# Performance work log

Hardware: AMD Instinct MI355X
Metric: run time of the kernel (lower is better)

The kernel has to match this reference:

```python
import jax, jax.numpy as jnp
import numpy as np

ALPHA = 0.2  # leaky relu negative slope (LinearNet default)


def _init_linear(key, fan_in, fan_out):
    kw, kb = jax.random.split(key)
    lim = 1.0 / np.sqrt(fan_in)
    W = jax.random.uniform(kw, (fan_in, fan_out), jnp.float32, -lim, lim)
    b = jax.random.uniform(kb, (fan_out,), jnp.float32, -lim, lim)
    return W, b


def setup_inputs() -> dict:
    key = jax.random.key(0)
    keys = jax.random.split(key, 8)
    B, N, F = 8, 512, 32
    x = jax.random.normal(keys[0], (B, N, F), jnp.float32)
    # fe: [2F=64 -> 64 -> 64 -> 64], all layers leaky-relu (final_linear=False)
    fe_W0, fe_b0 = _init_linear(keys[1], 2 * F, 64)
    fe_W1, fe_b1 = _init_linear(keys[2], 64, 64)
    fe_W2, fe_b2 = _init_linear(keys[3], 64, 64)
    # fn: [64 + F = 96 -> 128 -> 128 -> 32], last layer linear (final_linear=True)
    fn_W0, fn_b0 = _init_linear(keys[4], 64 + F, 128)
    fn_W1, fn_b1 = _init_linear(keys[5], 128, 128)
    fn_W2, fn_b2 = _init_linear(keys[6], 128, 32)
    return {
        "x": x,
        "fe_W0": fe_W0, "fe_b0": fe_b0,
        "fe_W1": fe_W1, "fe_b1": fe_b1,
        "fe_W2": fe_W2, "fe_b2": fe_b2,
        "fn_W0": fn_W0, "fn_b0": fn_b0,
        "fn_W1": fn_W1, "fn_b1": fn_b1,
        "fn_W2": fn_W2, "fn_b2": fn_b2,
    }


def reference(x, fe_W0, fe_b0, fe_W1, fe_b1, fe_W2, fe_b2,
              fn_W0, fn_b0, fn_W1, fn_b1, fn_W2, fn_b2):
    B, N, F = x.shape
    # all-pairs edge inputs: A[b,i,j] = concat(x[b,i], x[b,j])  (x1=repeat rows, x2=tile)
    xi = jnp.broadcast_to(x[:, :, None, :], (B, N, N, F))
    xj = jnp.broadcast_to(x[:, None, :, :], (B, N, N, F))
    A = jnp.concatenate([xi, xj], axis=-1)  # [B, N, N, 2F]
    # edge MLP fe: leaky relu after every layer (final_linear=False)
    for W, b in ((fe_W0, fe_b0), (fe_W1, fe_b1), (fe_W2, fe_b2)):
        A = jax.nn.leaky_relu(A @ W + b, negative_slope=ALPHA)
    # sum aggregation over the sender axis j
    agg = jnp.sum(A, axis=2)  # [B, N, K]
    h = jnp.concatenate([agg, x], axis=-1)  # [B, N, K + F]
    # node MLP fn: leaky relu on hidden layers, final layer linear
    h = jax.nn.leaky_relu(h @ fn_W0 + fn_b0, negative_slope=ALPHA)
    h = jax.nn.leaky_relu(h @ fn_W1 + fn_b1, negative_slope=ALPHA)
    out = h @ fn_W2 + fn_b2  # [B, N, output_node_size]
    return out
```

## Files before the change

### kernel.cpp

```cpp
#include <hip/hip_runtime.h>
#include <hip/hip_bf16.h>

#define ALPHA 0.2f
static __device__ __forceinline__ float lrel(float x) { return fmaxf(x, ALPHA * x); }

typedef __attribute__((ext_vector_type(8))) short bf16x8;
typedef __attribute__((ext_vector_type(4))) float f32x4;

union FragU { bf16x8 v; unsigned int u[4]; uint4 q; };

static __device__ __forceinline__ unsigned int pk2(float a, float b) {
    unsigned int r;
    asm("v_cvt_pk_bf16_f32 %0, %1, %2" : "=v"(r) : "v"(a), "v"(b));
    return r;
}
static __device__ __forceinline__ unsigned int cvl2(float a, float b) {
    return pk2(lrel(a), lrel(b));
}
static __device__ __forceinline__ unsigned short f2bf(float x) {
    union { float f; unsigned int u; } c;
    c.f = x;
    unsigned int r = c.u + 0x7FFFu + ((c.u >> 16) & 1u);
    return (unsigned short)(r >> 16);
}
static __device__ __forceinline__ int pi64(int s) {
    return 32 * ((s >> 4) >> 1) + 8 * ((s >> 2) & 3) + 4 * ((s >> 4) & 1) + (s & 3);
}

__global__ __launch_bounds__(256) void k_uv(
    const float* __restrict__ x, const float* __restrict__ W0, const float* __restrict__ b0,
    const float* __restrict__ W1, const float* __restrict__ W2,
    float* __restrict__ Upi, unsigned short* __restrict__ xbf, unsigned int* __restrict__ WF)
{
    if (blockIdx.x == 1024) {
        const int t = threadIdx.x;
        const int l = t & 63, part = t >> 6;
        const int lo = l & 15, g = l >> 4;
        for (int ff = part; ff < 20; ff += 4) {
            unsigned int o[4];
            if (ff < 4) {
                const int nf = ff;
                const int pc = 32 * (nf >> 1) + 8 * (lo >> 2) + 4 * (nf & 1) + (lo & 3);
#pragma unroll
                for (int uq = 0; uq < 4; ++uq) {
                    const int k0 = 8 * g + 2 * uq;
                    o[uq] = pk2(W0[(32 + k0) * 64 + pc], W0[(33 + k0) * 64 + pc]);
                }
            } else if (ff < 12) {
                const int s = (ff - 4) >> 2, nf = (ff - 4) & 3;
                const int pc = 32 * (nf >> 1) + 8 * (lo >> 2) + 4 * (nf & 1) + (lo & 3);
#pragma unroll
                for (int uq = 0; uq < 4; ++uq) {
                    const int k0 = 32 * s + 8 * g + 2 * uq;
                    o[uq] = pk2(W1[k0 * 64 + pc], W1[(k0 + 1) * 64 + pc]);
                }
            } else {
                const int s = (ff - 12) >> 2, nf = (ff - 12) & 3;
                const int c2 = 16 * nf + lo;
#pragma unroll
                for (int uq = 0; uq < 4; ++uq) {
                    const int k0 = 32 * s + 8 * g + 2 * uq;
                    o[uq] = pk2(W2[k0 * 64 + c2], W2[(k0 + 1) * 64 + c2]);
                }
            }
            *(uint4*)(WF + (ff * 64 + l) * 4) = make_uint4(o[0], o[1], o[2], o[3]);
        }
        return;
    }
    const int idx = blockIdx.x * 256 + threadIdx.x;
    const int n = idx >> 6;
    const int slot = idx & 63;
    const int f = pi64(slot);
    const float* xr = x + n * 32;
    float u = b0[f];
#pragma unroll
    for (int i = 0; i < 32; ++i) u += xr[i] * W0[i * 64 + f];
    Upi[idx] = u;
    if (slot < 32) xbf[n * 32 + slot] = f2bf(xr[slot]);
}

__global__ __launch_bounds__(256, 3) void k_edge(
    const float* __restrict__ Upi, const unsigned short* __restrict__ xbf,
    const unsigned int* __restrict__ WF,
    const float* __restrict__ b1, const float* __restrict__ b2,
    float* __restrict__ AGG)
{
    __shared__ uint4 wlds[1024];
    const int tid = threadIdx.x;
    const int w = tid >> 6, l = tid & 63;
    const int lo = l & 15, g = l >> 4;
    const int bid = blockIdx.x;
    const int b = bid >> 7, ig = bid & 127;
    const int node = b * 512 + ig * 4 + w;

    for (int idx = tid; idx < 1024; idx += 256)
        wlds[idx] = ((const uint4*)WF)[256 + idx];

    FragU w0f[4];
    const uint4* wp = (const uint4*)WF;
#pragma unroll
    for (int nf = 0; nf < 4; ++nf) w0f[nf].q = wp[nf * 64 + l];

    f32x4 u0f[4], b1f[4], b2f[4];
#pragma unroll
    for (int nf = 0; nf < 4; ++nf) {
        const float4 t0 = *(const float4*)(Upi + node * 64 + nf * 16 + 4 * g);
        u0f[nf] = (f32x4){t0.x, t0.y, t0.z, t0.w};
        const float4 t1 = *(const float4*)(b1 + 32 * (nf >> 1) + 8 * g + 4 * (nf & 1));
        const float4 t2 = *(const float4*)(b2 + 16 * nf + 4 * g);
        b1f[nf] = (f32x4){t1.x, t1.y, t1.z, t1.w};
        b2f[nf] = (f32x4){t2.x, t2.y, t2.z, t2.w};
    }

    const unsigned short* xb = xbf + b * 512 * 32;

    FragU xjT0, xjB;
    xjT0.q = *(const uint4*)(xb + lo * 32 + 8 * g);
    xjB.q  = *(const uint4*)(xb + (16 + lo) * 32 + 8 * g);

    __syncthreads();

    f32x4 acc0c[4];
#pragma unroll
    for (int nf = 0; nf < 4; ++nf)
        acc0c[nf] = __builtin_amdgcn_mfma_f32_16x16x32_bf16(w0f[nf].v, xjT0.v, u0f[nf], 0, 0, 0);

    f32x4 acc2p[4];
#pragma unroll
    for (int nf = 0; nf < 4; ++nf) { f32x4 z = {0.f, 0.f, 0.f, 0.f}; acc2p[nf] = z; }

    float aggL[4][4];
#pragma unroll
    for (int nf = 0; nf < 4; ++nf)
#pragma unroll
        for (int r = 0; r < 4; ++r) aggL[nf][r] = 0.f;

#pragma unroll 2
    for (int k = 0; k < 32; ++k) {
        int widx = 0;
        asm volatile("" : "+v"(widx));

        const int jn = ((k + 2) & 31) * 16;
        FragU xjn;
        xjn.q = *(const uint4*)(xb + (jn + lo) * 32 + 8 * g);

        __builtin_amdgcn_s_setprio(1);
        f32x4 acc0n[4];
#pragma unroll
        for (int nf = 0; nf < 4; ++nf)
            acc0n[nf] = __builtin_amdgcn_mfma_f32_16x16x32_bf16(w0f[nf].v, xjB.v, u0f[nf], 0, 0, 0);
        __builtin_amdgcn_s_setprio(0);

        FragU q0, q1;
        q0.u[0] = cvl2(acc0c[0][0], acc0c[0][1]);
        q0.u[1] = cvl2(acc0c[0][2], acc0c[0][3]);
        q0.u[2] = cvl2(acc0c[1][0], acc0c[1][1]);
        q0.u[3] = cvl2(acc0c[1][2], acc0c[1][3]);
        q1.u[0] = cvl2(acc0c[2][0], acc0c[2][1]);
        q1.u[1] = cvl2(acc0c[2][2], acc0c[2][3]);
        q1.u[2] = cvl2(acc0c[3][0], acc0c[3][1]);
        q1.u[3] = cvl2(acc0c[3][2], acc0c[3][3]);

        __builtin_amdgcn_s_setprio(1);
        f32x4 acc1[4];
#pragma unroll
        for (int nf = 0; nf < 4; ++nf) {
            FragU wa, wb;
            wa.q = wlds[widx + nf * 64 + l];
            wb.q = wlds[widx + (4 + nf) * 64 + l];
            acc1[nf] = __builtin_amdgcn_mfma_f32_16x16x32_bf16(wa.v, q0.v, b1f[nf], 0, 0, 0);
            acc1[nf] = __builtin_amdgcn_mfma_f32_16x16x32_bf16(wb.v, q1.v, acc1[nf], 0, 0, 0);
        }
        __builtin_amdgcn_s_setprio(0);

#pragma unroll
        for (int nf = 0; nf < 4; ++nf)
#pragma unroll
            for (int r = 0; r < 4; ++r) aggL[nf][r] += lrel(acc2p[nf][r]);

        FragU p0, p1;
        p0.u[0] = cvl2(acc1[0][0], acc1[0][1]);
        p0.u[1] = cvl2(acc1[0][2], acc1[0][3]);
        p0.u[2] = cvl2(acc1[1][0], acc1[1][1]);
        p0.u[3] = cvl2(acc1[1][2], acc1[1][3]);
        p1.u[0] = cvl2(acc1[2][0], acc1[2][1]);
        p1.u[1] = cvl2(acc1[2][2], acc1[2][3]);
        p1.u[2] = cvl2(acc1[3][0], acc1[3][1]);
        p1.u[3] = cvl2(acc1[3][2], acc1[3][3]);

        __builtin_amdgcn_s_setprio(1);
#pragma unroll
        for (int nf = 0; nf < 4; ++nf) {
            FragU wa, wb;
            wa.q = wlds[widx + (8 + nf) * 64 + l];
            wb.q = wlds[widx + (12 + nf) * 64 + l];
            acc2p[nf] = __builtin_amdgcn_mfma_f32_16x16x32_bf16(wa.v, p0.v, b2f[nf], 0, 0, 0);
            acc2p[nf] = __builtin_amdgcn_mfma_f32_16x16x32_bf16(wb.v, p1.v, acc2p[nf], 0, 0, 0);
        }
        __builtin_amdgcn_s_setprio(0);

#pragma unroll
        for (int nf = 0; nf < 4; ++nf) acc0c[nf] = acc0n[nf];
        xjB = xjn;
    }

#pragma unroll
    for (int nf = 0; nf < 4; ++nf)
#pragma unroll
        for (int r = 0; r < 4; ++r) aggL[nf][r] += lrel(acc2p[nf][r]);

#pragma unroll
    for (int nf = 0; nf < 4; ++nf)
#pragma unroll
        for (int r = 0; r < 4; ++r) {
            float v = aggL[nf][r];
            v += __shfl_xor(v, 1);
            v += __shfl_xor(v, 2);
            v += __shfl_xor(v, 4);
            v += __shfl_xor(v, 8);
            aggL[nf][r] = v;
        }
    if (lo == 0) {
#pragma unroll
        for (int nf = 0; nf < 4; ++nf) {
            float4 o = {aggL[nf][0], aggL[nf][1], aggL[nf][2], aggL[nf][3]};
            *(float4*)(AGG + node * 64 + 16 * nf + 4 * g) = o;
        }
    }
}

__global__ __launch_bounds__(256) void k_fn(
    const float* __restrict__ AGG, const float* __restrict__ x,
    const float* __restrict__ W0, const float* __restrict__ b0,
    const float* __restrict__ W1, const float* __restrict__ b1,
    const float* __restrict__ W2, const float* __restrict__ b2,
    float* __restrict__ out)
{
    __shared__ float in96T[96][8];
    __shared__ float h1T[128][8];
    __shared__ float h2T[128][8];
    const int t = threadIdx.x;
    const int half = t >> 7, f = t & 127;
    const int node0 = blockIdx.x * 8;

    for (int idx = t; idx < 768; idx += 256) {
        int nn = idx & 7, k = idx >> 3;
        in96T[k][nn] = (k < 64) ? AGG[(node0 + nn) * 64 + k]
                                : x[(node0 + nn) * 32 + (k - 64)];
    }
    __syncthreads();

    {
        float a0 = b0[f], a1 = a0, a2 = a0, a3 = a0;
#pragma unroll 4
        for (int k = 0; k < 96; ++k) {
            const float4 iv = *(const float4*)(&in96T[k][4 * half]);
            const float wv = W0[k * 128 + f];
            a0 += iv.x * wv; a1 += iv.y * wv; a2 += iv.z * wv; a3 += iv.w * wv;
        }
        float4 o = {lrel(a0), lrel(a1), lrel(a2), lrel(a3)};
        *(float4*)(&h1T[f][4 * half]) = o;
    }
    __syncthreads();

    {
        float a0 = b1[f], a1 = a0, a2 = a0, a3 = a0;
#pragma unroll 4
        for (int k = 0; k < 128; ++k) {
            const float4 iv = *(const float4*)(&h1T[k][4 * half]);
            const float wv = W1[k * 128 + f];
            a0 += iv.x * wv; a1 += iv.y * wv; a2 += iv.z * wv; a3 += iv.w * wv;
        }
        float4 o = {lrel(a0), lrel(a1), lrel(a2), lrel(a3)};
        *(float4*)(&h2T[f][4 * half]) = o;
    }
    __syncthreads();

    {
        const int nn = t >> 5, fo = t & 31;
        float a = b2[fo];
#pragma unroll 4
        for (int k = 0; k < 128; ++k) a += h2T[k][nn] * W2[k * 32 + fo];
        out[(node0 + nn) * 32 + fo] = a;
    }
}

extern "C" void kernel_launch(void* const* d_in, const int* in_sizes, int n_in,
                              void* d_out, int out_size, void* d_ws, size_t ws_size,
                              hipStream_t stream)
{
    const float* x    = (const float*)d_in[0];
    const float* feW0 = (const float*)d_in[1];
    const float* feb0 = (const float*)d_in[2];
    const float* feW1 = (const float*)d_in[3];
    const float* feb1 = (const float*)d_in[4];
    const float* feW2 = (const float*)d_in[5];
    const float* feb2 = (const float*)d_in[6];
    const float* fnW0 = (const float*)d_in[7];
    const float* fnb0 = (const float*)d_in[8];
    const float* fnW1 = (const float*)d_in[9];
    const float* fnb1 = (const float*)d_in[10];
    const float* fnW2 = (const float*)d_in[11];
    const float* fnb2 = (const float*)d_in[12];
    float* out = (float*)d_out;

    float* Upi = (float*)d_ws;
    float* AGG = Upi + 262144;
    unsigned short* xbf = (unsigned short*)(AGG + 262144);
    unsigned int* WF = (unsigned int*)(xbf + 131072);

    hipLaunchKernelGGL(k_uv,   dim3(1025), dim3(256), 0, stream, x, feW0, feb0, feW1, feW2, Upi, xbf, WF);
    hipLaunchKernelGGL(k_edge, dim3(1024), dim3(256), 0, stream, Upi, xbf, WF, feb1, feb2, AGG);
    hipLaunchKernelGGL(k_fn,   dim3(512),  dim3(256), 0, stream, AGG, x, fnW0, fnb0, fnW1, fnb1, fnW2, fnb2, out);
}
```

Measured before the change: 81.27 us.

## Interleave two j-tiles per iteration with inline-asm MFMA and fused leaky-relu aggregation

Restructures the edge loop to process two 16-wide sender tiles (A and B) per iteration, interleaving their MFMA chains so independent matrix ops hide each other's latency. The previous software pipeline (layer-0 MFMA one tile ahead, layer-2 activation one iteration behind) is dropped. MFMAs are now issued through inline asm with explicit accumulate constraints, and the leaky-relu sum is rewritten as 0.6x + 0.4|x| via two FMAs. Occupancy drops from 3 to 2 blocks per SM to make room for the extra live registers, and inline asm may limit how the compiler schedules instructions.

```diff
diff --git a/kernel.cpp b/kernel.cpp
--- a/kernel.cpp
+++ b/kernel.cpp
@@ -8,6 +8,15 @@
 typedef __attribute__((ext_vector_type(4))) float f32x4;
 
 union FragU { bf16x8 v; unsigned int u[4]; uint4 q; };
+
+static __device__ __forceinline__ f32x4 mfma_init(bf16x8 a, bf16x8 b, f32x4 c) {
+    f32x4 d;
+    asm("v_mfma_f32_16x16x32_bf16 %0, %1, %2, %3" : "=&v"(d) : "v"(a), "v"(b), "v"(c));
+    return d;
+}
+static __device__ __forceinline__ void mfma_acc(f32x4& acc, bf16x8 a, bf16x8 b) {
+    asm("v_mfma_f32_16x16x32_bf16 %0, %1, %2, %0" : "+v"(acc) : "v"(a), "v"(b));
+}
 
 static __device__ __forceinline__ unsigned int pk2(float a, float b) {
     unsigned int r;
@@ -16,6 +25,9 @@
 }
 static __device__ __forceinline__ unsigned int cvl2(float a, float b) {
     return pk2(lrel(a), lrel(b));
+}
+static __device__ __forceinline__ void aggfma(float& agg, float x) {
+    agg = fmaf(0.6f, x, fmaf(0.4f, fabsf(x), agg));
 }
 static __device__ __forceinline__ unsigned short f2bf(float x) {
     union { float f; unsigned int u; } c;
@@ -79,7 +91,7 @@
     if (slot < 32) xbf[n * 32 + slot] = f2bf(xr[slot]);
 }
 
-__global__ __launch_bounds__(256, 3) void k_edge(
+__global__ __launch_bounds__(256, 2) void k_edge(
     const float* __restrict__ Upi, const unsigned short* __restrict__ xbf,
     const unsigned int* __restrict__ WF,
     const float* __restrict__ b1, const float* __restrict__ b2,
@@ -114,100 +126,113 @@
 
     const unsigned short* xb = xbf + b * 512 * 32;
 
-    FragU xjT0, xjB;
-    xjT0.q = *(const uint4*)(xb + lo * 32 + 8 * g);
-    xjB.q  = *(const uint4*)(xb + (16 + lo) * 32 + 8 * g);
+    FragU xjA, xjB;
+    xjA.q = *(const uint4*)(xb + lo * 32 + 8 * g);
+    xjB.q = *(const uint4*)(xb + (16 + lo) * 32 + 8 * g);
+
+    float aggL[4][4];
+#pragma unroll
+    for (int nf = 0; nf < 4; ++nf)
+#pragma unroll
+        for (int r = 0; r < 4; ++r) aggL[nf][r] = 0.f;
 
     __syncthreads();
 
-    f32x4 acc0c[4];
-#pragma unroll
-    for (int nf = 0; nf < 4; ++nf)
-        acc0c[nf] = __builtin_amdgcn_mfma_f32_16x16x32_bf16(w0f[nf].v, xjT0.v, u0f[nf], 0, 0, 0);
-
-    f32x4 acc2p[4];
-#pragma unroll
-    for (int nf = 0; nf < 4; ++nf) { f32x4 z = {0.f, 0.f, 0.f, 0.f}; acc2p[nf] = z; }
-
-    float aggL[4][4];
-#pragma unroll
-    for (int nf = 0; nf < 4; ++nf)
-#pragma unroll
-        for (int r = 0; r < 4; ++r) aggL[nf][r] = 0.f;
-
-#pragma unroll 2
-    for (int k = 0; k < 32; ++k) {
+#pragma unroll 1
+    for (int k = 0; k < 16; ++k) {
         int widx = 0;
         asm volatile("" : "+v"(widx));
 
-        const int jn = ((k + 2) & 31) * 16;
-        FragU xjn;
-        xjn.q = *(const uint4*)(xb + (jn + lo) * 32 + 8 * g);
+        const int jA = ((2 * k + 2) & 31) * 16;
+        const int jB = ((2 * k + 3) & 31) * 16;
+        FragU xjAn, xjBn;
+        xjAn.q = *(const uint4*)(xb + (jA + lo) * 32 + 8 * g);
+        xjBn.q = *(const uint4*)(xb + (jB + lo) * 32 + 8 * g);
 
         __builtin_amdgcn_s_setprio(1);
-        f32x4 acc0n[4];
-#pragma unroll
-        for (int nf = 0; nf < 4; ++nf)
-            acc0n[nf] = __builtin_amdgcn_mfma_f32_16x16x32_bf16(w0f[nf].v, xjB.v, u0f[nf], 0, 0, 0);
+        f32x4 acc0A[4], acc0B[4];
+#pragma unroll
+        for (int nf = 0; nf < 4; ++nf) {
+            acc0A[nf] = mfma_init(w0f[nf].v, xjA.v, u0f[nf]);
+            acc0B[nf] = mfma_init(w0f[nf].v, xjB.v, u0f[nf]);
+        }
         __builtin_amdgcn_s_setprio(0);
 
-        FragU q0, q1;
-        q0.u[0] = cvl2(acc0c[0][0], acc0c[0][1]);
-        q0.u[1] = cvl2(acc0c[0][2], acc0c[0][3]);
-        q0.u[2] = cvl2(acc0c[1][0], acc0c[1][1]);
-        q0.u[3] = cvl2(acc0c[1][2], acc0c[1][3]);
-        q1.u[0] = cvl2(acc0c[2][0], acc0c[2][1]);
-        q1.u[1] = cvl2(acc0c[2][2], acc0c[2][3]);
-        q1.u[2] = cvl2(acc0c[3][0], acc0c[3][1]);
-        q1.u[3] = cvl2(acc0c[3][2], acc0c[3][3]);
+        FragU qA0, qA1, qB0, qB1;
+        qA0.u[0] = cvl2(acc0A[0][0], acc0A[0][1]);
+        qA0.u[1] = cvl2(acc0A[0][2], acc0A[0][3]);
+        qA0.u[2] = cvl2(acc0A[1][0], acc0A[1][1]);
+        qA0.u[3] = cvl2(acc0A[1][2], acc0A[1][3]);
+        qA1.u[0] = cvl2(acc0A[2][0], acc0A[2][1]);
+        qA1.u[1] = cvl2(acc0A[2][2], acc0A[2][3]);
+        qA1.u[2] = cvl2(acc0A[3][0], acc0A[3][1]);
+        qA1.u[3] = cvl2(acc0A[3][2], acc0A[3][3]);
+        qB0.u[0] = cvl2(acc0B[0][0], acc0B[0][1]);
+        qB0.u[1] = cvl2(acc0B[0][2], acc0B[0][3]);
+        qB0.u[2] = cvl2(acc0B[1][0], acc0B[1][1]);
+        qB0.u[3] = cvl2(acc0B[1][2], acc0B[1][3]);
+        qB1.u[0] = cvl2(acc0B[2][0], acc0B[2][1]);
+        qB1.u[1] = cvl2(acc0B[2][2], acc0B[2][3]);
+        qB1.u[2] = cvl2(acc0B[3][0], acc0B[3][1]);
+        qB1.u[3] = cvl2(acc0B[3][2], acc0B[3][3]);
 
         __builtin_amdgcn_s_setprio(1);
-        f32x4 acc1[4];
+        f32x4 acc1A[4], acc1B[4];
 #pragma unroll
         for (int nf = 0; nf < 4; ++nf) {
             FragU wa, wb;
             wa.q = wlds[widx + nf * 64 + l];
             wb.q = wlds[widx + (4 + nf) * 64 + l];
-            acc1[nf] = __builtin_amdgcn_mfma_f32_16x16x32_bf16(wa.v, q0.v, b1f[nf], 0, 0, 0);
-            acc1[nf] = __builtin_amdgcn_mfma_f32_16x16x32_bf16(wb.v, q1.v, acc1[nf], 0, 0, 0);
+            acc1A[nf] = mfma_init(wa.v, qA0.v, b1f[nf]);
+            acc1B[nf] = mfma_init(wa.v, qB0.v, b1f[nf]);
+            mfma_acc(acc1A[nf], wb.v, qA1.v);
+            mfma_acc(acc1B[nf], wb.v, qB1.v);
         }
         __builtin_amdgcn_s_setprio(0);
 
-#pragma unroll
-        for (int nf = 0; nf < 4; ++nf)
-#pragma unroll
-            for (int r = 0; r < 4; ++r) aggL[nf][r] += lrel(acc2p[nf][r]);
-
-        FragU p0, p1;
-        p0.u[0] = cvl2(acc1[0][0], acc1[0][1]);
-        p0.u[1] = cvl2(acc1[0][2], acc1[0][3]);
-        p0.u[2] = cvl2(acc1[1][0], acc1[1][1]);
-        p0.u[3] = cvl2(acc1[1][2], acc1[1][3]);
-        p1.u[0] = cvl2(acc1[2][0], acc1[2][1]);
-        p1.u[1] = cvl2(acc1[2][2], acc1[2][3]);
-        p1.u[2] = cvl2(acc1[3][0], acc1[3][1]);
-        p1.u[3] = cvl2(acc1[3][2], acc1[3][3]);
+        FragU pA0, pA1, pB0, pB1;
+        pA0.u[0] = cvl2(acc1A[0][0], acc1A[0][1]);
+        pA0.u[1] = cvl2(acc1A[0][2], acc1A[0][3]);
+        pA0.u[2] = cvl2(acc1A[1][0], acc1A[1][1]);
+        pA0.u[3] = cvl2(acc1A[1][2], acc1A[1][3]);
+        pA1.u[0] = cvl2(acc1A[2][0], acc1A[2][1]);
+        pA1.u[1] = cvl2(acc1A[2][2], acc1A[2][3]);
+        pA1.u[2] = cvl2(acc1A[3][0], acc1A[3][1]);
+        pA1.u[3] = cvl2(acc1A[3][2], acc1A[3][3]);
+        pB0.u[0] = cvl2(acc1B[0][0], acc1B[0][1]);
+        pB0.u[1] = cvl2(acc1B[0][2], acc1B[0][3]);
+        pB0.u[2] = cvl2(acc1B[1][0], acc1B[1][1]);
+        pB0.u[3] = cvl2(acc1B[1][2], acc1B[1][3]);
+        pB1.u[0] = cvl2(acc1B[2][0], acc1B[2][1]);
+        pB1.u[1] = cvl2(acc1B[2][2], acc1B[2][3]);
+        pB1.u[2] = cvl2(acc1B[3][0], acc1B[3][1]);
+        pB1.u[3] = cvl2(acc1B[3][2], acc1B[3][3]);
 
         __builtin_amdgcn_s_setprio(1);
+        f32x4 acc2A[4], acc2B[4];
 #pragma unroll
         for (int nf = 0; nf < 4; ++nf) {
             FragU wa, wb;
             wa.q = wlds[widx + (8 + nf) * 64 + l];
             wb.q = wlds[widx + (12 + nf) * 64 + l];
-            acc2p[nf] = __builtin_amdgcn_mfma_f32_16x16x32_bf16(wa.v, p0.v, b2f[nf], 0, 0, 0);
-            acc2p[nf] = __builtin_amdgcn_mfma_f32_16x16x32_bf16(wb.v, p1.v, acc2p[nf], 0, 0, 0);
+            acc2A[nf] = mfma_init(wa.v, pA0.v, b2f[nf]);
+            acc2B[nf] = mfma_init(wa.v, pB0.v, b2f[nf]);
+            mfma_acc(acc2A[nf], wb.v, pA1.v);
+            mfma_acc(acc2B[nf], wb.v, pB1.v);
         }
         __builtin_amdgcn_s_setprio(0);
 
 #pragma unroll
-        for (int nf = 0; nf < 4; ++nf) acc0c[nf] = acc0n[nf];
-        xjB = xjn;
-    }
-
-#pragma unroll
-    for (int nf = 0; nf < 4; ++nf)
-#pragma unroll
-        for (int r = 0; r < 4; ++r) aggL[nf][r] += lrel(acc2p[nf][r]);
+        for (int nf = 0; nf < 4; ++nf)
+#pragma unroll
+            for (int r = 0; r < 4; ++r) {
+                aggfma(aggL[nf][r], acc2A[nf][r]);
+                aggfma(aggL[nf][r], acc2B[nf][r]);
+            }
+
+        xjA = xjAn;
+        xjB = xjBn;
+    }
 
 #pragma unroll
     for (int nf = 0; nf < 4; ++nf)
```

Result: faster. 76.01 us (-6.5%).
